# Kernel tuning notes

Hardware: AMD Instinct MI355X
Metric: run time of the kernel (lower is better)

## Reference

```python
import jax, jax.numpy as jnp
import numpy as np

N = 100000       # nodes
E = 1600000      # edges
NFEAT, NHID, NCLASS = 512, 256, 40
NLAYERS = 10     # APPNP propagation steps K
ALPHA = 0.1      # teleport probability


def setup_inputs() -> dict:
    key = jax.random.key(0)
    ks = jax.random.split(key, 8)
    x = jax.random.normal(ks[0], (N, NFEAT), jnp.float32)
    row = jax.random.randint(ks[1], (E,), 0, N, jnp.int32)
    col = jax.random.randint(ks[2], (E,), 0, N, jnp.int32)
    vals = jax.random.uniform(ks[3], (E,), jnp.float32)
    # MyLinear init: uniform(-stdv, stdv) with stdv = 1/sqrt(in_features);
    # bias is a shape-[1] scalar (faithful to torch.FloatTensor([out_features])).
    s1 = 1.0 / np.sqrt(NFEAT)
    s2 = 1.0 / np.sqrt(NHID)
    W1 = jax.random.uniform(ks[4], (NFEAT, NHID), jnp.float32, -s1, s1)
    b1 = jax.random.uniform(ks[5], (1,), jnp.float32, -s1, s1)
    W2 = jax.random.uniform(ks[6], (NHID, NCLASS), jnp.float32, -s2, s2)
    b2 = jax.random.uniform(ks[7], (1,), jnp.float32, -s2, s2)
    return dict(x=x, row=row, col=col, vals=vals, W1=W1, b1=b1, W2=W2, b2=b2)


def reference(x, row, col, vals, W1, b1, W2, b2):
    # 2-layer MLP (eval mode: dropout inactive, no BN)
    h = jax.nn.relu(x @ W1 + b1)          # [N, NHID]
    h = h @ W2 + b2                        # [N, NCLASS]

    # sparse adjacency spmm via edge-list segment sum
    def spmm(z):
        return jax.ops.segment_sum(vals[:, None] * z[col], row, num_segments=N)

    # APPNP propagation: z <- (1-alpha) * A z + alpha * h
    def step(z, _):
        z = (1.0 - ALPHA) * spmm(z) + ALPHA * h
        return z, None

    z, _ = jax.lax.scan(step, h, None, length=NLAYERS)
    return jax.nn.log_softmax(z, axis=1)
```

## Files before the change

### kernel.cpp

```cpp
#include <hip/hip_runtime.h>


typedef unsigned short ushort_t;
typedef short short8 __attribute__((ext_vector_type(8)));
typedef float f32x4 __attribute__((ext_vector_type(4)));

#define NFEAT 512
#define NHID 256
#define NCLASS 40

static __device__ __forceinline__ float b2f(ushort_t u) {
    unsigned v = ((unsigned)u) << 16;
    float f;
    __builtin_memcpy(&f, &v, 4);
    return f;
}
static __device__ __forceinline__ ushort_t f2b(float f) {
    unsigned u;
    __builtin_memcpy(&u, &f, 4);
    unsigned r = u + 0x7FFFu + ((u >> 16) & 1u);
    return (ushort_t)(r >> 16);
}
static __device__ __forceinline__ ushort_t san_u(ushort_t u) {
    return ((u & 0x7F80u) == 0x7F80u) ? (ushort_t)0 : u;
}
static __device__ __forceinline__ float ldmix(const void* p, size_t i, int isbf) {
    if (isbf) return b2f(san_u(((const ushort_t*)p)[i]));
    return ((const float*)p)[i];
}
static __device__ __forceinline__ float ldz(const void* p, size_t i, int zbf) {
    return zbf ? b2f(((const ushort_t*)p)[i]) : ((const float*)p)[i];
}
static __device__ __forceinline__ void stz(void* p, size_t i, int zbf, float v) {
    if (zbf) ((ushort_t*)p)[i] = f2b(v);
    else ((float*)p)[i] = v;
}

__global__ void detect_kernel(const ushort_t* __restrict__ x, int* __restrict__ flag) {
    __shared__ int cnt_s;
    if (threadIdx.x == 0) cnt_s = 0;
    __syncthreads();
    int c = 0;
    for (int i = threadIdx.x; i < 2048; i += 256) {
        ushort_t u = x[2 * i];
        int e = (u >> 7) & 0xFF;
        if (e >= 107 && e <= 141) c++;
    }
    atomicAdd(&cnt_s, c);
    __syncthreads();
    if (threadIdx.x == 0) flag[0] = (cnt_s >= 1024) ? 1 : 0;
}


__global__ void zero_kernel(int* __restrict__ p, int n) {
    int i = blockIdx.x * 256 + threadIdx.x;
    if (i < n) p[i] = 0;
}

__global__ void hist_kernel(const int* __restrict__ row, int* __restrict__ deg, int e, int n) {
    int i = blockIdx.x * 256 + threadIdx.x;
    if (i < e) {
        int r = row[i];
        if ((unsigned)r < (unsigned)n) atomicAdd(&deg[r], 1);
    }
}

__global__ void scan_blocksum(const int* __restrict__ deg, int* __restrict__ bsum, int n) {
    __shared__ int s[256];
    int t = threadIdx.x;
    int i = blockIdx.x * 256 + t;
    s[t] = (i < n) ? deg[i] : 0;
    __syncthreads();
    for (int o = 128; o; o >>= 1) {
        if (t < o) s[t] += s[t + o];
        __syncthreads();
    }
    if (t == 0) bsum[blockIdx.x] = s[0];
}

__global__ void scan_bsum_excl(int* __restrict__ bsum, int nb) {
    __shared__ int s[512];
    int t = threadIdx.x;
    int v = (t < nb) ? bsum[t] : 0;
    int own = v;
    s[t] = v;
    __syncthreads();
    for (int o = 1; o < 512; o <<= 1) {
        int add = (t >= o) ? s[t - o] : 0;
        __syncthreads();
        s[t] += add;
        __syncthreads();
    }
    if (t < nb) bsum[t] = s[t] - own;
}

__global__ void scan_emit(const int* __restrict__ deg, const int* __restrict__ bsum,
                          int* __restrict__ row_start, int* __restrict__ cursor, int n) {
    __shared__ int s[256];
    int t = threadIdx.x;
    int i = blockIdx.x * 256 + t;
    int v = (i < n) ? deg[i] : 0;
    int own = v;
    s[t] = v;
    __syncthreads();
    for (int o = 1; o < 256; o <<= 1) {
        int add = (t >= o) ? s[t - o] : 0;
        __syncthreads();
        s[t] += add;
        __syncthreads();
    }
    if (i < n) {
        int rs = bsum[blockIdx.x] + s[t] - own;
        row_start[i] = rs;
        cursor[i] = rs;
    }
}

__global__ void scatter_kernel(const int* __restrict__ row, const int* __restrict__ col,
                               const void* __restrict__ vals, int* __restrict__ cursor,
                               int* __restrict__ cs_col, void* __restrict__ cs_val,
                               const int* __restrict__ flag, int zbf, int e, int n) {
    int i = blockIdx.x * 256 + threadIdx.x;
    if (i < e) {
        int isbf = flag[0];
        int r = row[i];
        if ((unsigned)r >= (unsigned)n) return;
        int p = atomicAdd(&cursor[r], 1);
        if ((unsigned)p < (unsigned)e) {
            int c = col[i];
            cs_col[p] = ((unsigned)c < (unsigned)n) ? c : 0;
            stz(cs_val, p, zbf, ldmix(vals, i, isbf));
        }
    }
}


__global__ void w1frag_kernel(const void* __restrict__ W1, ushort_t* __restrict__ w1f,
                              const int* __restrict__ flag) {
    int t = blockIdx.x * 256 + threadIdx.x;
    if (t >= 16 * 16 * 64) return;
    int isbf = flag[0];
    int l = t & 63, nt = (t >> 6) & 15, kb = t >> 10;
    ushort_t tmp[8];
#pragma unroll
    for (int j = 0; j < 8; j++) {
        int k = kb * 32 + (l >> 4) * 8 + j;
        int nn = nt * 16 + (l & 15);
        tmp[j] = f2b(ldmix(W1, (size_t)k * NHID + nn, isbf));
    }
    *(short8*)(w1f + (size_t)t * 8) = *(short8*)tmp;
}

__global__ void w2frag_kernel(const void* __restrict__ W2, ushort_t* __restrict__ w2f,
                              const int* __restrict__ flag) {
    int t = blockIdx.x * 256 + threadIdx.x;
    if (t >= 8 * 3 * 64) return;
    int isbf = flag[0];
    int l = t % 64;
    int nt = (t / 64) % 3;
    int kb = t / 192;
    ushort_t tmp[8];
#pragma unroll
    for (int j = 0; j < 8; j++) {
        int k = kb * 32 + (l >> 4) * 8 + j;
        int nn = nt * 16 + (l & 15);
        tmp[j] = (nn < NCLASS) ? f2b(ldmix(W2, (size_t)k * NCLASS + nn, isbf)) : (ushort_t)0;
    }
    *(short8*)(w2f + (size_t)t * 8) = *(short8*)tmp;
}


__global__ __launch_bounds__(256) void mlp_kernel(const void* __restrict__ x,
                                                  const ushort_t* __restrict__ w1f,
                                                  const ushort_t* __restrict__ w2f,
                                                  const void* __restrict__ b1,
                                                  const void* __restrict__ b2,
                                                  void* __restrict__ h,
                                                  const int* __restrict__ flag, int zbf, int n) {
    __shared__ ushort_t Alds[64][40];
    __shared__ ushort_t Hlds[64][264];
    const int t = threadIdx.x;
    const int isbf = flag[0];
    const int wv = t >> 6, l = t & 63;
    const int lq = l >> 4, lr = l & 15;
    const int m0 = blockIdx.x * 64;

    f32x4 acc[16];
#pragma unroll
    for (int i = 0; i < 16; i++) acc[i] = (f32x4){0.f, 0.f, 0.f, 0.f};

    const int rS = t >> 2, qS = t & 3;
    int rowS = m0 + rS;
    if (rowS > n - 1) rowS = n - 1;
    const size_t xbase = (size_t)rowS * NFEAT + qS * 8;
    const ushort_t* aldsp = &Alds[wv * 16 + lr][lq * 8];

    for (int kb = 0; kb < 16; kb++) {
        short8 av;
        if (isbf) {
            av = *(const short8*)((const ushort_t*)x + xbase + kb * 32);
#pragma unroll
            for (int j = 0; j < 8; j++) {
                ushort_t u = (ushort_t)av[j];
                if ((u & 0x7F80u) == 0x7F80u) av[j] = 0;
            }
        } else {
            const float* xf = (const float*)x + xbase + kb * 32;
            f32x4 a0 = *(const f32x4*)xf;
            f32x4 a1 = *(const f32x4*)(xf + 4);
#pragma unroll
            for (int j = 0; j < 4; j++) {
                av[j] = (short)f2b(a0[j]);
                av[4 + j] = (short)f2b(a1[j]);
            }
        }
        *(short8*)&Alds[rS][qS * 8] = av;
        __syncthreads();
        short8 afrag = *(const short8*)aldsp;
        const ushort_t* bp = w1f + ((size_t)(kb * 16) * 64 + l) * 8;
#pragma unroll
        for (int nt = 0; nt < 16; nt++) {
            short8 bfrag = *(const short8*)(bp + (size_t)nt * 64 * 8);
            acc[nt] = __builtin_amdgcn_mfma_f32_16x16x32_bf16(afrag, bfrag, acc[nt], 0, 0, 0);
        }
        __syncthreads();
    }

    float bias1 = ldmix(b1, 0, isbf);
#pragma unroll
    for (int nt = 0; nt < 16; nt++) {
#pragma unroll
        for (int i = 0; i < 4; i++) {
            float v = acc[nt][i] + bias1;
            v = fmaxf(v, 0.f);
            Hlds[wv * 16 + lq * 4 + i][nt * 16 + lr] = f2b(v);
        }
    }
    __syncthreads();

    f32x4 acc2[3];
#pragma unroll
    for (int i = 0; i < 3; i++) acc2[i] = (f32x4){0.f, 0.f, 0.f, 0.f};
    const ushort_t* hp = &Hlds[wv * 16 + lr][lq * 8];
#pragma unroll
    for (int kb = 0; kb < 8; kb++) {
        short8 afrag = *(const short8*)(hp + kb * 32);
#pragma unroll
        for (int nt = 0; nt < 3; nt++) {
            short8 bfrag = *(const short8*)(w2f + ((size_t)(kb * 3 + nt) * 64 + l) * 8);
            acc2[nt] = __builtin_amdgcn_mfma_f32_16x16x32_bf16(afrag, bfrag, acc2[nt], 0, 0, 0);
        }
    }

    float bias2 = ldmix(b2, 0, isbf);
#pragma unroll
    for (int nt = 0; nt < 3; nt++) {
#pragma unroll
        for (int i = 0; i < 4; i++) {
            int rowg = m0 + wv * 16 + lq * 4 + i;
            int colg = nt * 16 + lr;
            if (rowg < n && colg < NCLASS)
                stz(h, (size_t)rowg * NCLASS + colg, zbf, acc2[nt][i] + bias2);
        }
    }
}


template <int ZBF>
__global__ __launch_bounds__(256) void prop_kernel(const void* __restrict__ zin,
                                                   void* __restrict__ zout,
                                                   const void* __restrict__ h,
                                                   const int* __restrict__ row_start,
                                                   const int* __restrict__ deg,
                                                   const int* __restrict__ cs_col,
                                                   const void* __restrict__ cs_val, int n) {
    int w = blockIdx.x * 4 + (threadIdx.x >> 6);
    int lane = threadIdx.x & 63;
    if (w >= n) return;
    int start = row_start[w];
    int d = deg[w];
    const bool laneok = lane < NCLASS;
    float acc = 0.f;
    for (int base = 0; base < d; base += 64) {
        int m = d - base;
        if (m > 64) m = 64;
        int c = 0;
        float v = 0.f;
        if (lane < m) {
            size_t idx = (size_t)start + base + lane;
            c = cs_col[idx];
            v = ZBF ? b2f(((const ushort_t*)cs_val)[idx]) : ((const float*)cs_val)[idx];
        }
        for (int j = 0; j < m; j += 8) {
            int cc[8];
            float vv[8];
#pragma unroll
            for (int k = 0; k < 8; k++) {
                cc[k] = __shfl(c, j + k);
                vv[k] = __shfl(v, j + k);
            }
            if (laneok) {
                float zv[8];
#pragma unroll
                for (int k = 0; k < 8; k++) {
                    size_t zi = (size_t)cc[k] * NCLASS + lane;
                    zv[k] = ZBF ? b2f(((const ushort_t*)zin)[zi]) : ((const float*)zin)[zi];
                }
#pragma unroll
                for (int k = 0; k < 8; k++) acc += vv[k] * zv[k];
            }
        }
    }
    if (laneok) {
        float hv = ZBF ? b2f(((const ushort_t*)h)[(size_t)w * NCLASS + lane])
                       : ((const float*)h)[(size_t)w * NCLASS + lane];
        float r = 0.9f * acc + 0.1f * hv;
        if (ZBF) ((ushort_t*)zout)[(size_t)w * NCLASS + lane] = f2b(r);
        else ((float*)zout)[(size_t)w * NCLASS + lane] = r;
    }
}


__global__ __launch_bounds__(256) void lsm_kernel(const void* __restrict__ z,
                                                  void* __restrict__ out,
                                                  const int* __restrict__ flag, int zbf, int n) {
    int w = blockIdx.x * 4 + (threadIdx.x >> 6);
    int lane = threadIdx.x & 63;
    if (w >= n) return;
    int isbf = flag[0];
    float v = (lane < NCLASS) ? ldz(z, (size_t)w * NCLASS + lane, zbf) : -INFINITY;
    float m = v;
    for (int o = 32; o; o >>= 1) m = fmaxf(m, __shfl_xor(m, o));
    float e = (lane < NCLASS) ? __expf(v - m) : 0.f;
    float s = e;
    for (int o = 32; o; o >>= 1) s += __shfl_xor(s, o);
    if (lane < NCLASS) {
        float r = v - m - __logf(s);
        if (isbf) ((ushort_t*)out)[(size_t)w * NCLASS + lane] = f2b(r);
        else ((float*)out)[(size_t)w * NCLASS + lane] = r;
    }
}


extern "C" void kernel_launch(void* const* d_in, const int* in_sizes, int n_in, void* d_out,
                              int out_size, void* d_ws, size_t ws_size, hipStream_t stream) {
    const void* x = d_in[0];
    const int* row = (const int*)d_in[1];
    const int* col = (const int*)d_in[2];
    const void* vals = d_in[3];
    const void* W1 = d_in[4];
    const void* b1 = d_in[5];
    const void* W2 = d_in[6];
    const void* b2 = d_in[7];

    const int N = in_sizes[0] / NFEAT;
    const int E = in_sizes[1];

    const int roomy = (ws_size == 0) || (ws_size >= (size_t)66 * 1024 * 1024);
    const int zbf = roomy ? 0 : 1;
    const size_t ez = roomy ? 4 : 2;

    char* ws = (char*)d_ws;
    size_t off = 0;
    auto take = [&](size_t bytes) {
        size_t o = off;
        off = (off + bytes + 255) & ~(size_t)255;
        return (void*)(ws + o);
    };
    void* h = take((size_t)N * NCLASS * ez);
    void* zA = take((size_t)N * NCLASS * ez);
    void* zB = take((size_t)N * NCLASS * ez);
    int* cs_col = (int*)take((size_t)E * 4);
    void* cs_val = take((size_t)E * ez);
    int* deg = (int*)take((size_t)N * 4);
    int* row_start = (int*)take((size_t)N * 4);
    int* cursor = (int*)take((size_t)N * 4);
    ushort_t* w1f = (ushort_t*)take((size_t)NFEAT * NHID * 2);
    ushort_t* w2f = (ushort_t*)take((size_t)8 * 3 * 64 * 8 * 2);
    int* bsum = (int*)take(512 * 4);
    int* flag = (int*)take(256);

    const int NB = (N + 255) / 256;
    const int EB = (E + 255) / 256;
    const int GB = (N + 63) / 64;
    const int PB = (N + 3) / 4;

    detect_kernel<<<1, 256, 0, stream>>>((const ushort_t*)x, flag);

    zero_kernel<<<(N + 255) / 256, 256, 0, stream>>>(deg, N);
    hist_kernel<<<EB, 256, 0, stream>>>(row, deg, E, N);
    scan_blocksum<<<NB, 256, 0, stream>>>(deg, bsum, N);
    scan_bsum_excl<<<1, 512, 0, stream>>>(bsum, NB);
    scan_emit<<<NB, 256, 0, stream>>>(deg, bsum, row_start, cursor, N);
    scatter_kernel<<<EB, 256, 0, stream>>>(row, col, vals, cursor, cs_col, cs_val, flag, zbf, E,
                                           N);

    w1frag_kernel<<<64, 256, 0, stream>>>(W1, w1f, flag);
    w2frag_kernel<<<6, 256, 0, stream>>>(W2, w2f, flag);

    mlp_kernel<<<GB, 256, 0, stream>>>(x, w1f, w2f, b1, b2, h, flag, zbf, N);

    if (zbf) {
        prop_kernel<1><<<PB, 256, 0, stream>>>(h, zA, h, row_start, deg, cs_col, cs_val, N);
        const void* zi = zA;
        void* zo = zB;
        for (int s = 1; s < 10; s++) {
            prop_kernel<1><<<PB, 256, 0, stream>>>(zi, zo, h, row_start, deg, cs_col, cs_val, N);
            const void* tmp = zi;
            zi = zo;
            zo = (void*)tmp;
        }
        lsm_kernel<<<PB, 256, 0, stream>>>(zi, d_out, flag, zbf, N);
    } else {
        prop_kernel<0><<<PB, 256, 0, stream>>>(h, zA, h, row_start, deg, cs_col, cs_val, N);
        const void* zi = zA;
        void* zo = zB;
        for (int s = 1; s < 10; s++) {
            prop_kernel<0><<<PB, 256, 0, stream>>>(zi, zo, h, row_start, deg, cs_col, cs_val, N);
            const void* tmp = zi;
            zi = zo;
            zo = (void*)tmp;
        }
        lsm_kernel<<<PB, 256, 0, stream>>>(zi, d_out, flag, zbf, N);
    }
}
```

Baseline: 1.140 ms.

## Restructure MLP GEMM1 into 2x2 wave tiling with register-prefetched fragments

Replaces the LDS-staged A tile and per-k-step barriers in the first MLP GEMM with direct global loads of A fragments into registers. Each wave now computes a 32x128 sub-tile, so every B fragment feeds two MFMAs. The next k-step's A and B fragments are loaded before the current MFMAs run, and the isbf branch is hoisted into template instantiations. The aim is to remove syncthreads stalls, halve W1 global reads per MFMA, and hide load latency, at the cost of more registers under a launch_bounds occupancy hint of 3.

```diff
diff --git a/kernel.cpp b/kernel.cpp
--- a/kernel.cpp
+++ b/kernel.cpp
@@ -170,72 +170,110 @@
 }
 
 
-__global__ __launch_bounds__(256) void mlp_kernel(const void* __restrict__ x,
-                                                  const ushort_t* __restrict__ w1f,
-                                                  const ushort_t* __restrict__ w2f,
-                                                  const void* __restrict__ b1,
-                                                  const void* __restrict__ b2,
-                                                  void* __restrict__ h,
-                                                  const int* __restrict__ flag, int zbf, int n) {
-    __shared__ ushort_t Alds[64][40];
+template <int ISBF>
+static __device__ __forceinline__ short8 load_afrag(const void* __restrict__ x, size_t base) {
+    short8 av;
+    if (ISBF) {
+        av = *(const short8*)((const ushort_t*)x + base);
+#pragma unroll
+        for (int j = 0; j < 8; j++) {
+            ushort_t u = (ushort_t)av[j];
+            if ((u & 0x7F80u) == 0x7F80u) av[j] = 0;
+        }
+    } else {
+        const float* xf = (const float*)x + base;
+        f32x4 a0 = *(const f32x4*)xf;
+        f32x4 a1 = *(const f32x4*)(xf + 4);
+#pragma unroll
+        for (int j = 0; j < 4; j++) {
+            av[j] = (short)f2b(a0[j]);
+            av[4 + j] = (short)f2b(a1[j]);
+        }
+    }
+    return av;
+}
+
+template <int ISBF>
+static __device__ __forceinline__ void gemm1_loop(const void* __restrict__ x,
+                                                  const ushort_t* __restrict__ w1base,
+                                                  size_t abase0, size_t abase1,
+                                                  f32x4 (&acc)[2][8]) {
+    short8 a0 = load_afrag<ISBF>(x, abase0);
+    short8 a1 = load_afrag<ISBF>(x, abase1);
+    short8 b[8];
+#pragma unroll
+    for (int nn = 0; nn < 8; nn++) b[nn] = *(const short8*)(w1base + (size_t)nn * 512);
+#pragma unroll
+    for (int kb = 0; kb < 16; kb++) {
+        short8 na0 = a0, na1 = a1;
+        short8 nb[8];
+        if (kb < 15) {
+            na0 = load_afrag<ISBF>(x, abase0 + (size_t)(kb + 1) * 32);
+            na1 = load_afrag<ISBF>(x, abase1 + (size_t)(kb + 1) * 32);
+            const ushort_t* bk = w1base + (size_t)(kb + 1) * 8192;
+#pragma unroll
+            for (int nn = 0; nn < 8; nn++) nb[nn] = *(const short8*)(bk + (size_t)nn * 512);
+        }
+#pragma unroll
+        for (int nn = 0; nn < 8; nn++) {
+            acc[0][nn] = __builtin_amdgcn_mfma_f32_16x16x32_bf16(a0, b[nn], acc[0][nn], 0, 0, 0);
+            acc[1][nn] = __builtin_amdgcn_mfma_f32_16x16x32_bf16(a1, b[nn], acc[1][nn], 0, 0, 0);
+        }
+        if (kb < 15) {
+            a0 = na0;
+            a1 = na1;
+#pragma unroll
+            for (int nn = 0; nn < 8; nn++) b[nn] = nb[nn];
+        }
+    }
+}
+
+__global__ __launch_bounds__(256, 3) void mlp_kernel(const void* __restrict__ x,
+                                                     const ushort_t* __restrict__ w1f,
+                                                     const ushort_t* __restrict__ w2f,
+                                                     const void* __restrict__ b1,
+                                                     const void* __restrict__ b2,
+                                                     void* __restrict__ h,
+                                                     const int* __restrict__ flag, int zbf,
+                                                     int n) {
     __shared__ ushort_t Hlds[64][264];
     const int t = threadIdx.x;
     const int isbf = flag[0];
     const int wv = t >> 6, l = t & 63;
     const int lq = l >> 4, lr = l & 15;
+    const int wr = wv >> 1, wc = wv & 1;
     const int m0 = blockIdx.x * 64;
 
-    f32x4 acc[16];
-#pragma unroll
-    for (int i = 0; i < 16; i++) acc[i] = (f32x4){0.f, 0.f, 0.f, 0.f};
-
-    const int rS = t >> 2, qS = t & 3;
-    int rowS = m0 + rS;
-    if (rowS > n - 1) rowS = n - 1;
-    const size_t xbase = (size_t)rowS * NFEAT + qS * 8;
-    const ushort_t* aldsp = &Alds[wv * 16 + lr][lq * 8];
-
-    for (int kb = 0; kb < 16; kb++) {
-        short8 av;
-        if (isbf) {
-            av = *(const short8*)((const ushort_t*)x + xbase + kb * 32);
-#pragma unroll
-            for (int j = 0; j < 8; j++) {
-                ushort_t u = (ushort_t)av[j];
-                if ((u & 0x7F80u) == 0x7F80u) av[j] = 0;
+    int rowA0 = m0 + wr * 32 + lr;
+    int rowA1 = rowA0 + 16;
+    if (rowA0 > n - 1) rowA0 = n - 1;
+    if (rowA1 > n - 1) rowA1 = n - 1;
+    const size_t abase0 = (size_t)rowA0 * NFEAT + (size_t)lq * 8;
+    const size_t abase1 = (size_t)rowA1 * NFEAT + (size_t)lq * 8;
+    const ushort_t* w1base = w1f + (size_t)wc * 4096 + (size_t)l * 8;
+
+    f32x4 acc[2][8];
+#pragma unroll
+    for (int r = 0; r < 2; r++)
+#pragma unroll
+        for (int nn = 0; nn < 8; nn++) acc[r][nn] = (f32x4){0.f, 0.f, 0.f, 0.f};
+
+    if (isbf)
+        gemm1_loop<1>(x, w1base, abase0, abase1, acc);
+    else
+        gemm1_loop<0>(x, w1base, abase0, abase1, acc);
+
+    float bias1 = ldmix(b1, 0, isbf);
+#pragma unroll
+    for (int r = 0; r < 2; r++)
+#pragma unroll
+        for (int nn = 0; nn < 8; nn++)
+#pragma unroll
+            for (int i = 0; i < 4; i++) {
+                float v = acc[r][nn][i] + bias1;
+                v = fmaxf(v, 0.f);
+                Hlds[wr * 32 + r * 16 + lq * 4 + i][wc * 128 + nn * 16 + lr] = f2b(v);
             }
-        } else {
-            const float* xf = (const float*)x + xbase + kb * 32;
-            f32x4 a0 = *(const f32x4*)xf;
-            f32x4 a1 = *(const f32x4*)(xf + 4);
-#pragma unroll
-            for (int j = 0; j < 4; j++) {
-                av[j] = (short)f2b(a0[j]);
-                av[4 + j] = (short)f2b(a1[j]);
-            }
-        }
-        *(short8*)&Alds[rS][qS * 8] = av;
-        __syncthreads();
-        short8 afrag = *(const short8*)aldsp;
-        const ushort_t* bp = w1f + ((size_t)(kb * 16) * 64 + l) * 8;
-#pragma unroll
-        for (int nt = 0; nt < 16; nt++) {
-            short8 bfrag = *(const short8*)(bp + (size_t)nt * 64 * 8);
-            acc[nt] = __builtin_amdgcn_mfma_f32_16x16x32_bf16(afrag, bfrag, acc[nt], 0, 0, 0);
-        }
-        __syncthreads();
-    }
-
-    float bias1 = ldmix(b1, 0, isbf);
-#pragma unroll
-    for (int nt = 0; nt < 16; nt++) {
-#pragma unroll
-        for (int i = 0; i < 4; i++) {
-            float v = acc[nt][i] + bias1;
-            v = fmaxf(v, 0.f);
-            Hlds[wv * 16 + lq * 4 + i][nt * 16 + lr] = f2b(v);
-        }
-    }
     __syncthreads();
 
     f32x4 acc2[3];
```

Result: no change. 1.124 ms (-1.4%).
